# Kernel optimization log

Hardware: AMD Instinct MI355X
Metric: run time of the kernel (lower is better)

## Reference

```python
import jax, jax.numpy as jnp
import numpy as np

NUM_HEADS = 32
HEAD_DIM = 128
HIDDEN = 4096
MAX_SEQ = 4096
B, S = 8, 16
POS = 2048


def setup_inputs() -> dict:
    key = jax.random.key(0)
    ks = jax.random.split(key, 7)
    sc = 1.0 / np.sqrt(HIDDEN)
    return {
        "h": jax.random.normal(ks[0], (B, S, HIDDEN), dtype=jnp.float32),
        "Wq": jax.random.normal(ks[1], (HIDDEN, HIDDEN), dtype=jnp.float32) * sc,
        "Wk": jax.random.normal(ks[2], (HIDDEN, HIDDEN), dtype=jnp.float32) * sc,
        "Wv": jax.random.normal(ks[3], (HIDDEN, HIDDEN), dtype=jnp.float32) * sc,
        "Wo": jax.random.normal(ks[4], (HIDDEN, HIDDEN), dtype=jnp.float32) * sc,
        "K_cache": jax.random.normal(ks[5], (B, NUM_HEADS, MAX_SEQ, HEAD_DIM), dtype=jnp.float32),
        "V_cache": jax.random.normal(ks[6], (B, NUM_HEADS, MAX_SEQ, HEAD_DIM), dtype=jnp.float32),
        "pos": POS,
    }


def reference(h, Wq, Wk, Wv, Wo, K_cache, V_cache, pos):
    b, s, _ = h.shape
    # QKV projections (Linear with weight [out, in], no bias): h @ W.T
    def proj(W):
        return (h @ W.T).reshape(b, s, NUM_HEADS, HEAD_DIM).transpose(0, 2, 1, 3)  # [B,H,S,hd]
    Q, K, V = proj(Wq), proj(Wk), proj(Wv)
    # write new K/V into cache at [pos : pos+S] (pos is a static Python int)
    K_cache = K_cache.at[:, :, pos:pos + s, :].set(K)
    V_cache = V_cache.at[:, :, pos:pos + s, :].set(V)
    K_all = K_cache[:, :, :pos + s, :]  # [B,H,T,hd], T = pos+S
    V_all = V_cache[:, :, :pos + s, :]
    scores = jnp.einsum('bhsd,bhtd->bhst', Q, K_all) / np.sqrt(HEAD_DIM)  # [B,H,S,T]
    if s > 1:
        # causal mask applied only to the freshly-written block of columns
        causal = jnp.triu(jnp.full((s, s), -jnp.inf, dtype=scores.dtype), k=1)
        scores = scores.at[:, :, :, pos:pos + s].add(causal)
    attn = jax.nn.softmax(scores, axis=-1)
    out = jnp.einsum('bhst,bhtd->bhsd', attn, V_all)  # [B,H,S,hd]
    out = out.transpose(0, 2, 1, 3).reshape(b, s, NUM_HEADS * HEAD_DIM)
    return out @ Wo.T
```

## Files before the change

kernel.cpp:

```cpp
#include <hip/hip_runtime.h>

typedef _Float16 f16;
typedef _Float16 f16x8 __attribute__((ext_vector_type(8)));
typedef _Float16 f16x4 __attribute__((ext_vector_type(4)));
typedef _Float16 f16x2 __attribute__((ext_vector_type(2)));
typedef float f32x4 __attribute__((ext_vector_type(4)));
typedef float f32x2 __attribute__((ext_vector_type(2)));

#define MFMA16(a, b, c) __builtin_amdgcn_mfma_f32_16x16x32_f16(a, b, c, 0, 0, 0)

#define HID 4096
#define ROWS 128
#define SCL 0.12751743f

__device__ __forceinline__ f16x8 cvt8(float4 x, float4 y) {
    f16x8 v = {(f16)x.x, (f16)x.y, (f16)x.z, (f16)x.w,
               (f16)y.x, (f16)y.y, (f16)y.z, (f16)y.w};
    return v;
}

__device__ __forceinline__ int swz2(int row, int cb) {
    return row * 256 + (cb ^ ((row & 7) << 4));
}

__global__ void k_cvt(const float* __restrict__ src, f16* __restrict__ dst) {
    const int i = blockIdx.x * blockDim.x + threadIdx.x;
    const float4* s4 = (const float4*)src + (size_t)i * 2;
    float4 x = s4[0], y = s4[1];
    *((f16x8*)dst + i) = cvt8(x, y);
}

__global__ __launch_bounds__(256) void k_qproj(
        const f16* __restrict__ hb, const float* __restrict__ W,
        f16* __restrict__ Ob) {
    const int c0 = blockIdx.x * 16;

    __shared__ __align__(16) f16 sA[128 * 128];
    __shared__ __align__(16) f16 sB[16 * 128];

    const int tid = threadIdx.x;
    const int w = tid >> 6, l = tid & 63;
    const int rw = w * 32;
    const int ar = tid >> 4;
    const int ac = (tid & 15) * 8;

    f32x4 acc0 = {}, acc1 = {};

    float4 wx, wy;
    f16x8 hreg[8];
    {
        const float* wp = W + (size_t)(c0 + ar) * HID + ac;
        wx = *(const float4*)wp; wy = *(const float4*)(wp + 4);
        #pragma unroll
        for (int c = 0; c < 8; ++c)
            hreg[c] = *(const f16x8*)(hb + (size_t)(c * 16 + ar) * HID + ac);
    }

    for (int ks = 0; ks < 32; ++ks) {
        #pragma unroll
        for (int c = 0; c < 8; ++c)
            *(f16x8*)((char*)sA + swz2(c * 16 + ar, ac * 2)) = hreg[c];
        *(f16x8*)((char*)sB + swz2(ar, ac * 2)) = cvt8(wx, wy);
        __syncthreads();
        if (ks < 31) {
            const int k0 = (ks + 1) * 128;
            const float* wp = W + (size_t)(c0 + ar) * HID + k0 + ac;
            wx = *(const float4*)wp; wy = *(const float4*)(wp + 4);
            #pragma unroll
            for (int c = 0; c < 8; ++c)
                hreg[c] = *(const f16x8*)(hb + (size_t)(c * 16 + ar) * HID + k0 + ac);
        }
        #pragma unroll
        for (int kk = 0; kk < 4; ++kk) {
            const int cb = kk * 64 + (l >> 4) * 16;
            f16x8 a0 = *(const f16x8*)((char*)sA + swz2(rw + (l & 15), cb));
            f16x8 a1 = *(const f16x8*)((char*)sA + swz2(rw + 16 + (l & 15), cb));
            f16x8 b0 = *(const f16x8*)((char*)sB + swz2((l & 15), cb));
            acc0 = MFMA16(a0, b0, acc0);
            acc1 = MFMA16(a1, b0, acc1);
        }
        __syncthreads();
    }
    #pragma unroll
    for (int r = 0; r < 4; ++r) {
        const int col = c0 + (l & 15);
        Ob[(size_t)(rw + (l >> 4) * 4 + r) * HID + col]      = (f16)acc0[r];
        Ob[(size_t)(rw + 16 + (l >> 4) * 4 + r) * HID + col] = (f16)acc1[r];
    }
}

__global__ __launch_bounds__(512) void k_mega(
        const f16* __restrict__ hb,
        const float* __restrict__ Wk, const float* __restrict__ Wv,
        f16* __restrict__ Kw, f16* __restrict__ Vw,
        const f16* __restrict__ Qw,
        const float* __restrict__ Kc, const float* __restrict__ Vc,
        const int* __restrict__ posp,
        float* __restrict__ Pm, float* __restrict__ Pl, float* __restrict__ Po) {

    __shared__ __align__(16) char smem[65536 + 1024];
    const int tid = threadIdx.x, w = tid >> 6, l = tid & 63;

    if (blockIdx.x & 1) {
        const int pid = blockIdx.x >> 1;
        const float* __restrict__ W = (pid & 128) ? Wv : Wk;
        f16* __restrict__ Ob = (pid & 128) ? Vw : Kw;
        const int c0 = (pid & 127) * 32;

        f16* sA = (f16*)smem;
        f16* sB = (f16*)smem + 128 * 128;

        const int ar = tid >> 4;
        const int ac = (tid & 15) * 8;

        f32x4 acc0 = {}, acc1 = {};

        float4 wx, wy;
        f16x8 hreg[4];
        {
            const float* wp = W + (size_t)(c0 + ar) * HID + ac;
            wx = *(const float4*)wp; wy = *(const float4*)(wp + 4);
            #pragma unroll
            for (int c = 0; c < 4; ++c)
                hreg[c] = *(const f16x8*)(hb + (size_t)(c * 32 + ar) * HID + ac);
        }

        const int rw = (w >> 1) * 32;
        const int cw = (w & 1) * 16;

        for (int ks = 0; ks < 32; ++ks) {
            #pragma unroll
            for (int c = 0; c < 4; ++c)
                *(f16x8*)((char*)sA + swz2(c * 32 + ar, ac * 2)) = hreg[c];
            *(f16x8*)((char*)sB + swz2(ar, ac * 2)) = cvt8(wx, wy);
            __syncthreads();
            if (ks < 31) {
                const int k0 = (ks + 1) * 128;
                const float* wp = W + (size_t)(c0 + ar) * HID + k0 + ac;
                wx = *(const float4*)wp; wy = *(const float4*)(wp + 4);
                #pragma unroll
                for (int c = 0; c < 4; ++c)
                    hreg[c] = *(const f16x8*)(hb + (size_t)(c * 32 + ar) * HID + k0 + ac);
            }
            #pragma unroll
            for (int kk = 0; kk < 4; ++kk) {
                const int cb = kk * 64 + (l >> 4) * 16;
                f16x8 a0 = *(const f16x8*)((char*)sA + swz2(rw + (l & 15), cb));
                f16x8 a1 = *(const f16x8*)((char*)sA + swz2(rw + 16 + (l & 15), cb));
                f16x8 b0 = *(const f16x8*)((char*)sB + swz2(cw + (l & 15), cb));
                acc0 = MFMA16(a0, b0, acc0);
                acc1 = MFMA16(a1, b0, acc1);
            }
            __syncthreads();
        }
        #pragma unroll
        for (int r = 0; r < 4; ++r) {
            const int col = c0 + cw + (l & 15);
            Ob[(size_t)(rw + (l >> 4) * 4 + r) * HID + col]      = (f16)acc0[r];
            Ob[(size_t)(rw + 16 + (l >> 4) * 4 + r) * HID + col] = (f16)acc1[r];
        }
        return;
    }

    const int bh = blockIdx.x >> 1;
    const int b = bh >> 5, hh = bh & 31;
    const int pos = *posp;
    const int npure = pos >> 5;

    const float* Kb = Kc + (size_t)bh * (4096 * 128);
    const float* Vb = Vc + (size_t)bh * (4096 * 128);

    f16x8 qf[4];
    {
        const f16* qp = Qw + (size_t)(b * 16 + (l & 15)) * HID + hh * 128 + (l >> 4) * 8;
        #pragma unroll
        for (int kk = 0; kk < 4; ++kk) qf[kk] = *(const f16x8*)(qp + kk * 32);
    }

    f32x4 o[8] = {};
    float m[4], lsum[4];
    #pragma unroll
    for (int r = 0; r < 4; ++r) { m[r] = -3e38f; lsum[r] = 0.f; }

    f16* Pw = (f16*)smem + w * 640;

    const int start = (w * npure) >> 3;
    const int end   = ((w + 1) * npure) >> 3;
    for (int tau = start; tau < end; ++tau) {
        const int t0 = tau << 5;

        f16x8 kf[2][4];
        #pragma unroll
        for (int tn = 0; tn < 2; ++tn) {
            const float* kp = Kb + (size_t)(t0 + tn * 16 + (l & 15)) * 128 + (l >> 4) * 8;
            #pragma unroll
            for (int kk = 0; kk < 4; ++kk) {
                float4 x = *(const float4*)(kp + kk * 32);
                float4 y = *(const float4*)(kp + kk * 32 + 4);
                kf[tn][kk] = cvt8(x, y);
            }
        }
        f32x4 sa[2] = {};
        #pragma unroll
        for (int tn = 0; tn < 2; ++tn)
            #pragma unroll
            for (int kk = 0; kk < 4; ++kk) sa[tn] = MFMA16(qf[kk], kf[tn][kk], sa[tn]);

        f16x8 vf[8];
        {
            const float* vp = Vb + (size_t)(t0 + (l >> 4) * 8) * 128 + (l & 15);
            #pragma unroll
            for (int dt = 0; dt < 8; ++dt)
                #pragma unroll
                for (int j = 0; j < 8; ++j) vf[dt][j] = (f16)vp[j * 128 + dt * 16];
        }

        float sc[2][4];
        #pragma unroll
        for (int tn = 0; tn < 2; ++tn)
            #pragma unroll
            for (int r = 0; r < 4; ++r) sc[tn][r] = sa[tn][r] * SCL;
        float vmax[4];
        #pragma unroll
        for (int r = 0; r < 4; ++r) vmax[r] = fmaxf(sc[0][r], sc[1][r]);
        #pragma unroll
        for (int d = 1; d < 16; d <<= 1)
            #pragma unroll
            for (int r = 0; r < 4; ++r) vmax[r] = fmaxf(vmax[r], __shfl_xor(vmax[r], d));
        float p[2][4], rs[4], fac[4];
        #pragma unroll
        for (int r = 0; r < 4; ++r) {
            const float mn = fmaxf(m[r], vmax[r]);
            fac[r] = exp2f(m[r] - mn);
            m[r] = mn;
            p[0][r] = exp2f(sc[0][r] - mn);
            p[1][r] = exp2f(sc[1][r] - mn);
            rs[r] = p[0][r] + p[1][r];
            lsum[r] *= fac[r];
        }
        #pragma unroll
        for (int d = 1; d < 16; d <<= 1)
            #pragma unroll
            for (int r = 0; r < 4; ++r) rs[r] += __shfl_xor(rs[r], d);
        #pragma unroll
        for (int r = 0; r < 4; ++r) lsum[r] += rs[r];
        #pragma unroll
        for (int dt = 0; dt < 8; ++dt)
            #pragma unroll
            for (int r = 0; r < 4; ++r) o[dt][r] *= fac[r];

        #pragma unroll
        for (int r = 0; r < 4; ++r) {
            const int s_ = (l >> 4) * 4 + r;
            Pw[s_ * 40 + (l & 15)]      = (f16)p[0][r];
            Pw[s_ * 40 + 16 + (l & 15)] = (f16)p[1][r];
        }
        asm volatile("s_waitcnt lgkmcnt(0)" ::: "memory");
        f16x8 pa = *(const f16x8*)(Pw + (l & 15) * 40 + (l >> 4) * 8);

        #pragma unroll
        for (int dt = 0; dt < 8; ++dt) o[dt] = MFMA16(pa, vf[dt], o[dt]);
    }

    __syncthreads();
    float* Osh = (float*)smem;
    float* Msh = (float*)(smem + 65536);
    float* Lsh = Msh + 128;
    #pragma unroll
    for (int dt = 0; dt < 8; ++dt)
        #pragma unroll
        for (int r = 0; r < 4; ++r)
            Osh[w * 2048 + ((l >> 4) * 4 + r) * 128 + dt * 16 + (l & 15)] = o[dt][r];
    if ((l & 15) == 0) {
        #pragma unroll
        for (int r = 0; r < 4; ++r) {
            Msh[w * 16 + (l >> 4) * 4 + r] = m[r];
            Lsh[w * 16 + (l >> 4) * 4 + r] = lsum[r];
        }
    }
    __syncthreads();
    {
        const int s_ = tid >> 5;
        const int d_ = (tid & 31) * 4;
        float M = -3e38f;
        #pragma unroll
        for (int ww = 0; ww < 8; ++ww) M = fmaxf(M, Msh[ww * 16 + s_]);
        float L = 0.f;
        f32x4 oa = {};
        #pragma unroll
        for (int ww = 0; ww < 8; ++ww) {
            const float e = exp2f(Msh[ww * 16 + s_] - M);
            L += e * Lsh[ww * 16 + s_];
            f32x4 v = *(const f32x4*)(Osh + ww * 2048 + s_ * 128 + d_);
            #pragma unroll
            for (int r = 0; r < 4; ++r) oa[r] += e * v[r];
        }
        if ((tid & 31) == 0) {
            Pm[bh * 16 + s_] = M;
            Pl[bh * 16 + s_] = L;
        }
        *(f32x4*)(Po + (size_t)bh * 2048 + s_ * 128 + d_) = oa;
    }
}

__global__ __launch_bounds__(256) void k_fin(
        const f16* __restrict__ Qw, const f16* __restrict__ Kw,
        const f16* __restrict__ Vw,
        const float* __restrict__ Kc, const float* __restrict__ Vc,
        const int* __restrict__ posp,
        const float* __restrict__ Pm, const float* __restrict__ Pl,
        const float* __restrict__ Po, f16* __restrict__ Ow) {

    __shared__ float sP[16][48];
    __shared__ float sF[16], sL[16];

    const int bh = blockIdx.x, b = bh >> 5, hh = bh & 31;
    const int tid = threadIdx.x;
    const int pos = *posp;
    const int base = (pos >> 5) << 5;
    const int nb = pos + 16 - base;

    {
        const int s_ = tid >> 4, tt0 = tid & 15;
        const f16* qp = Qw + (size_t)(b * 16 + s_) * HID + hh * 128;
        const float m_p = Pm[bh * 16 + s_];
        const float l_p = Pl[bh * 16 + s_];

        float sc[3];
        float rowmax = -3e38f;
        #pragma unroll
        for (int it = 0; it < 3; ++it) {
            const int tt = it * 16 + tt0;
            float d = -3e38f;
            if (tt < nb) {
                const int t = base + tt;
                float acc = 0.f;
                if (t < pos) {
                    const float* kp = Kc + ((size_t)bh * 4096 + t) * 128;
                    #pragma unroll
                    for (int c = 0; c < 16; ++c) {
                        f16x8 q8 = *(const f16x8*)(qp + c * 8);
                        float4 ka = *(const float4*)(kp + c * 8);
                        float4 kb = *(const float4*)(kp + c * 8 + 4);
                        acc += (float)q8[0] * ka.x + (float)q8[1] * ka.y +
                               (float)q8[2] * ka.z + (float)q8[3] * ka.w +
                               (float)q8[4] * kb.x + (float)q8[5] * kb.y +
                               (float)q8[6] * kb.z + (float)q8[7] * kb.w;
                    }
                    d = acc * SCL;
                } else {
                    const f16* kp = Kw + (size_t)(b * 16 + (t - pos)) * HID + hh * 128;
                    #pragma unroll
                    for (int c = 0; c < 16; ++c) {
                        f16x8 q8 = *(const f16x8*)(qp + c * 8);
                        f16x8 k8 = *(const f16x8*)(kp + c * 8);
                        #pragma unroll
                        for (int j = 0; j < 8; ++j) acc += (float)q8[j] * (float)k8[j];
                    }
                    d = acc * SCL;
                    if ((t - pos) > s_) d = -3e38f;
                }
            }
            sc[it] = d;
            rowmax = fmaxf(rowmax, d);
        }
        #pragma unroll
        for (int dd = 1; dd < 16; dd <<= 1)
            rowmax = fmaxf(rowmax, __shfl_xor(rowmax, dd));

        const float M = fmaxf(m_p, rowmax);
        const float fac = exp2f(m_p - M);
        float ps = 0.f;
        #pragma unroll
        for (int it = 0; it < 3; ++it) {
            const float p = (sc[it] < -1e29f) ? 0.f : exp2f(sc[it] - M);
            ps += p;
            sP[s_][it * 16 + tt0] = p;
        }
        #pragma unroll
        for (int dd = 1; dd < 16; dd <<= 1) ps += __shfl_xor(ps, dd);
        if (tt0 == 0) {
            sF[s_] = fac;
            sL[s_] = fac * l_p + ps;
        }
    }
    __syncthreads();

    {
        const int s2 = tid >> 4;
        const int d0 = (tid & 15) * 8;
        const float f = sF[s2];
        float acc[8];
        const float* po = Po + (size_t)bh * 2048 + s2 * 128 + d0;
        #pragma unroll
        for (int j = 0; j < 8; ++j) acc[j] = f * po[j];

        for (int tt = 0; tt < nb; ++tt) {
            const float pv = sP[s2][tt];
            const int t = base + tt;
            if (t < pos) {
                const float* vp = Vc + ((size_t)bh * 4096 + t) * 128 + d0;
                float4 va = *(const float4*)vp;
                float4 vb = *(const float4*)(vp + 4);
                acc[0] += pv * va.x; acc[1] += pv * va.y;
                acc[2] += pv * va.z; acc[3] += pv * va.w;
                acc[4] += pv * vb.x; acc[5] += pv * vb.y;
                acc[6] += pv * vb.z; acc[7] += pv * vb.w;
            } else {
                const f16* vp = Vw + (size_t)(b * 16 + (t - pos)) * HID + hh * 128 + d0;
                f16x8 v8 = *(const f16x8*)vp;
                #pragma unroll
                for (int j = 0; j < 8; ++j) acc[j] += pv * (float)v8[j];
            }
        }
        const float inv = 1.f / sL[s2];
        f16x8 res;
        #pragma unroll
        for (int j = 0; j < 8; ++j) res[j] = (f16)(acc[j] * inv);
        *(f16x8*)(Ow + (size_t)(b * 16 + s2) * HID + hh * 128 + d0) = res;
    }
}

__global__ __launch_bounds__(256) void k_oproj(
        const f16* __restrict__ Oa, const float* __restrict__ Wo,
        float* __restrict__ out) {
    const int c0 = blockIdx.x * 16;

    __shared__ __align__(16) f16 sA[128 * 128];
    __shared__ __align__(16) f16 sB[16 * 128];

    const int tid = threadIdx.x;
    const int w = tid >> 6, l = tid & 63;
    const int rw = w * 32;
    const int ar = tid >> 4;
    const int ac = (tid & 15) * 8;

    f32x4 acc0 = {}, acc1 = {};

    float4 wx, wy;
    f16x8 hreg[8];
    {
        const float* wp = Wo + (size_t)(c0 + ar) * HID + ac;
        wx = *(const float4*)wp; wy = *(const float4*)(wp + 4);
        #pragma unroll
        for (int c = 0; c < 8; ++c)
            hreg[c] = *(const f16x8*)(Oa + (size_t)(c * 16 + ar) * HID + ac);
    }

    for (int ks = 0; ks < 32; ++ks) {
        #pragma unroll
        for (int c = 0; c < 8; ++c)
            *(f16x8*)((char*)sA + swz2(c * 16 + ar, ac * 2)) = hreg[c];
        *(f16x8*)((char*)sB + swz2(ar, ac * 2)) = cvt8(wx, wy);
        __syncthreads();
        if (ks < 31) {
            const int k0 = (ks + 1) * 128;
            const float* wp = Wo + (size_t)(c0 + ar) * HID + k0 + ac;
            wx = *(const float4*)wp; wy = *(const float4*)(wp + 4);
            #pragma unroll
            for (int c = 0; c < 8; ++c)
                hreg[c] = *(const f16x8*)(Oa + (size_t)(c * 16 + ar) * HID + k0 + ac);
        }
        #pragma unroll
        for (int kk = 0; kk < 4; ++kk) {
            const int cb = kk * 64 + (l >> 4) * 16;
            f16x8 a0 = *(const f16x8*)((char*)sA + swz2(rw + (l & 15), cb));
            f16x8 a1 = *(const f16x8*)((char*)sA + swz2(rw + 16 + (l & 15), cb));
            f16x8 b0 = *(const f16x8*)((char*)sB + swz2((l & 15), cb));
            acc0 = MFMA16(a0, b0, acc0);
            acc1 = MFMA16(a1, b0, acc1);
        }
        __syncthreads();
    }
    #pragma unroll
    for (int r = 0; r < 4; ++r) {
        const int col = c0 + (l & 15);
        out[(size_t)(rw + (l >> 4) * 4 + r) * HID + col]      = acc0[r];
        out[(size_t)(rw + 16 + (l >> 4) * 4 + r) * HID + col] = acc1[r];
    }
}

extern "C" void kernel_launch(void* const* d_in, const int* in_sizes, int n_in,
                              void* d_out, int out_size, void* d_ws, size_t ws_size,
                              hipStream_t stream) {
    const float* h  = (const float*)d_in[0];
    const float* Wq = (const float*)d_in[1];
    const float* Wk = (const float*)d_in[2];
    const float* Wv = (const float*)d_in[3];
    const float* Wo = (const float*)d_in[4];
    const float* Kc = (const float*)d_in[5];
    const float* Vc = (const float*)d_in[6];
    const int* pos  = (const int*)d_in[7];
    float* out = (float*)d_out;

    f16* hws = (f16*)d_ws;
    f16* Qw  = hws + ROWS * HID;
    f16* Kw  = Qw + ROWS * HID;
    f16* Vw  = Kw + ROWS * HID;
    f16* Ow  = Vw + ROWS * HID;
    float* Pm = (float*)(Ow + ROWS * HID);
    float* Pl = Pm + 256 * 16;
    float* Po = Pl + 256 * 16;

    k_cvt<<<256, 256, 0, stream>>>(h, hws);
    k_qproj<<<256, 256, 0, stream>>>(hws, Wq, Qw);
    k_mega<<<512, 512, 0, stream>>>(hws, Wk, Wv, Kw, Vw, Qw, Kc, Vc, pos, Pm, Pl, Po);
    k_fin<<<256, 256, 0, stream>>>(Qw, Kw, Vw, Kc, Vc, pos, Pm, Pl, Po, Ow);
    k_oproj<<<256, 256, 0, stream>>>(Ow, Wo, out);
}
```

Before: 229.1 us.

## Split K/V projection out of attention kernel and split attention over two blocks per head

The fused mega kernel, which interleaved K/V projection blocks with attention blocks, is split into two kernels. A single projection kernel now computes Q, K and V with 768 blocks. The attention kernel now gives each (batch, head) two blocks, each covering half of the cached sequence, and writes two partial softmax states. The finishing kernel merges both partials with rescaling. This spreads the cache-streaming attention across twice as many blocks, at the cost of an extra kernel boundary and a serial dependency between projection and attention.

```diff
diff --git a/kernel.cpp b/kernel.cpp
--- a/kernel.cpp
+++ b/kernel.cpp
@@ -30,10 +30,16 @@
     *((f16x8*)dst + i) = cvt8(x, y);
 }
 
-__global__ __launch_bounds__(256) void k_qproj(
-        const f16* __restrict__ hb, const float* __restrict__ W,
-        f16* __restrict__ Ob) {
-    const int c0 = blockIdx.x * 16;
+__global__ __launch_bounds__(256) void k_proj(
+        const f16* __restrict__ hb,
+        const float* __restrict__ Wq, const float* __restrict__ Wk,
+        const float* __restrict__ Wv,
+        f16* __restrict__ Qw, f16* __restrict__ Kw, f16* __restrict__ Vw) {
+    const int mat = blockIdx.x >> 8;
+    const int ct  = blockIdx.x & 255;
+    const float* __restrict__ W = (mat == 0) ? Wq : (mat == 1) ? Wk : Wv;
+    f16* __restrict__ Ob = (mat == 0) ? Qw : (mat == 1) ? Kw : Vw;
+    const int c0 = ct * 16;
 
     __shared__ __align__(16) f16 sA[128 * 128];
     __shared__ __align__(16) f16 sB[16 * 128];
@@ -89,83 +95,22 @@
     }
 }
 
-__global__ __launch_bounds__(512) void k_mega(
-        const f16* __restrict__ hb,
-        const float* __restrict__ Wk, const float* __restrict__ Wv,
-        f16* __restrict__ Kw, f16* __restrict__ Vw,
+__global__ __launch_bounds__(512) void k_attn(
         const f16* __restrict__ Qw,
         const float* __restrict__ Kc, const float* __restrict__ Vc,
         const int* __restrict__ posp,
         float* __restrict__ Pm, float* __restrict__ Pl, float* __restrict__ Po) {
 
     __shared__ __align__(16) char smem[65536 + 1024];
+
+    const int bh = blockIdx.x >> 1;
+    const int q  = blockIdx.x & 1;
+    const int b = bh >> 5, hh = bh & 31;
     const int tid = threadIdx.x, w = tid >> 6, l = tid & 63;
-
-    if (blockIdx.x & 1) {
-        const int pid = blockIdx.x >> 1;
-        const float* __restrict__ W = (pid & 128) ? Wv : Wk;
-        f16* __restrict__ Ob = (pid & 128) ? Vw : Kw;
-        const int c0 = (pid & 127) * 32;
-
-        f16* sA = (f16*)smem;
-        f16* sB = (f16*)smem + 128 * 128;
-
-        const int ar = tid >> 4;
-        const int ac = (tid & 15) * 8;
-
-        f32x4 acc0 = {}, acc1 = {};
-
-        float4 wx, wy;
-        f16x8 hreg[4];
-        {
-            const float* wp = W + (size_t)(c0 + ar) * HID + ac;
-            wx = *(const float4*)wp; wy = *(const float4*)(wp + 4);
-            #pragma unroll
-            for (int c = 0; c < 4; ++c)
-                hreg[c] = *(const f16x8*)(hb + (size_t)(c * 32 + ar) * HID + ac);
-        }
-
-        const int rw = (w >> 1) * 32;
-        const int cw = (w & 1) * 16;
-
-        for (int ks = 0; ks < 32; ++ks) {
-            #pragma unroll
-            for (int c = 0; c < 4; ++c)
-                *(f16x8*)((char*)sA + swz2(c * 32 + ar, ac * 2)) = hreg[c];
-            *(f16x8*)((char*)sB + swz2(ar, ac * 2)) = cvt8(wx, wy);
-            __syncthreads();
-            if (ks < 31) {
-                const int k0 = (ks + 1) * 128;
-                const float* wp = W + (size_t)(c0 + ar) * HID + k0 + ac;
-                wx = *(const float4*)wp; wy = *(const float4*)(wp + 4);
-                #pragma unroll
-                for (int c = 0; c < 4; ++c)
-                    hreg[c] = *(const f16x8*)(hb + (size_t)(c * 32 + ar) * HID + k0 + ac);
-            }
-            #pragma unroll
-            for (int kk = 0; kk < 4; ++kk) {
-                const int cb = kk * 64 + (l >> 4) * 16;
-                f16x8 a0 = *(const f16x8*)((char*)sA + swz2(rw + (l & 15), cb));
-                f16x8 a1 = *(const f16x8*)((char*)sA + swz2(rw + 16 + (l & 15), cb));
-                f16x8 b0 = *(const f16x8*)((char*)sB + swz2(cw + (l & 15), cb));
-                acc0 = MFMA16(a0, b0, acc0);
-                acc1 = MFMA16(a1, b0, acc1);
-            }
-            __syncthreads();
-        }
-        #pragma unroll
-        for (int r = 0; r < 4; ++r) {
-            const int col = c0 + cw + (l & 15);
-            Ob[(size_t)(rw + (l >> 4) * 4 + r) * HID + col]      = (f16)acc0[r];
-            Ob[(size_t)(rw + 16 + (l >> 4) * 4 + r) * HID + col] = (f16)acc1[r];
-        }
-        return;
-    }
-
-    const int bh = blockIdx.x >> 1;
-    const int b = bh >> 5, hh = bh & 31;
     const int pos = *posp;
     const int npure = pos >> 5;
+    const int nblk = npure >> 1;
+    const int tbase = q * nblk;
 
     const float* Kb = Kc + (size_t)bh * (4096 * 128);
     const float* Vb = Vc + (size_t)bh * (4096 * 128);
@@ -184,8 +129,8 @@
 
     f16* Pw = (f16*)smem + w * 640;
 
-    const int start = (w * npure) >> 3;
-    const int end   = ((w + 1) * npure) >> 3;
+    const int start = tbase + ((w * nblk) >> 3);
+    const int end   = tbase + (((w + 1) * nblk) >> 3);
     for (int tau = start; tau < end; ++tau) {
         const int t0 = tau << 5;
 
@@ -280,6 +225,7 @@
     }
     __syncthreads();
     {
+        const int pb = blockIdx.x;
         const int s_ = tid >> 5;
         const int d_ = (tid & 31) * 4;
         float M = -3e38f;
@@ -296,10 +242,10 @@
             for (int r = 0; r < 4; ++r) oa[r] += e * v[r];
         }
         if ((tid & 31) == 0) {
-            Pm[bh * 16 + s_] = M;
-            Pl[bh * 16 + s_] = L;
-        }
-        *(f32x4*)(Po + (size_t)bh * 2048 + s_ * 128 + d_) = oa;
+            Pm[pb * 16 + s_] = M;
+            Pl[pb * 16 + s_] = L;
+        }
+        *(f32x4*)(Po + (size_t)pb * 2048 + s_ * 128 + d_) = oa;
     }
 }
 
@@ -312,7 +258,7 @@
         const float* __restrict__ Po, f16* __restrict__ Ow) {
 
     __shared__ float sP[16][48];
-    __shared__ float sF[16], sL[16];
+    __shared__ float sF0[16], sF1[16], sL[16];
 
     const int bh = blockIdx.x, b = bh >> 5, hh = bh & 31;
     const int tid = threadIdx.x;
@@ -323,8 +269,10 @@
     {
         const int s_ = tid >> 4, tt0 = tid & 15;
         const f16* qp = Qw + (size_t)(b * 16 + s_) * HID + hh * 128;
-        const float m_p = Pm[bh * 16 + s_];
-        const float l_p = Pl[bh * 16 + s_];
+        const float m0 = Pm[(bh * 2) * 16 + s_];
+        const float m1 = Pm[(bh * 2 + 1) * 16 + s_];
+        const float l0 = Pl[(bh * 2) * 16 + s_];
+        const float l1 = Pl[(bh * 2 + 1) * 16 + s_];
 
         float sc[3];
         float rowmax = -3e38f;
@@ -368,8 +316,9 @@
         for (int dd = 1; dd < 16; dd <<= 1)
             rowmax = fmaxf(rowmax, __shfl_xor(rowmax, dd));
 
-        const float M = fmaxf(m_p, rowmax);
-        const float fac = exp2f(m_p - M);
+        const float M = fmaxf(fmaxf(m0, m1), rowmax);
+        const float f0 = exp2f(m0 - M);
+        const float f1 = exp2f(m1 - M);
         float ps = 0.f;
         #pragma unroll
         for (int it = 0; it < 3; ++it) {
@@ -380,8 +329,9 @@
         #pragma unroll
         for (int dd = 1; dd < 16; dd <<= 1) ps += __shfl_xor(ps, dd);
         if (tt0 == 0) {
-            sF[s_] = fac;
-            sL[s_] = fac * l_p + ps;
+            sF0[s_] = f0;
+            sF1[s_] = f1;
+            sL[s_] = f0 * l0 + f1 * l1 + ps;
         }
     }
     __syncthreads();
@@ -389,11 +339,12 @@
     {
         const int s2 = tid >> 4;
         const int d0 = (tid & 15) * 8;
-        const float f = sF[s2];
+        const float f0 = sF0[s2], f1 = sF1[s2];
         float acc[8];
-        const float* po = Po + (size_t)bh * 2048 + s2 * 128 + d0;
-        #pragma unroll
-        for (int j = 0; j < 8; ++j) acc[j] = f * po[j];
+        const float* po0 = Po + (size_t)(bh * 2) * 2048 + s2 * 128 + d0;
+        const float* po1 = Po + (size_t)(bh * 2 + 1) * 2048 + s2 * 128 + d0;
+        #pragma unroll
+        for (int j = 0; j < 8; ++j) acc[j] = f0 * po0[j] + f1 * po1[j];
 
         for (int tt = 0; tt < nb; ++tt) {
             const float pv = sP[s2][tt];
@@ -499,12 +450,12 @@
     f16* Vw  = Kw + ROWS * HID;
     f16* Ow  = Vw + ROWS * HID;
     float* Pm = (float*)(Ow + ROWS * HID);
-    float* Pl = Pm + 256 * 16;
-    float* Po = Pl + 256 * 16;
+    float* Pl = Pm + 512 * 16;
+    float* Po = Pl + 512 * 16;
 
     k_cvt<<<256, 256, 0, stream>>>(h, hws);
-    k_qproj<<<256, 256, 0, stream>>>(hws, Wq, Qw);
-    k_mega<<<512, 512, 0, stream>>>(hws, Wk, Wv, Kw, Vw, Qw, Kc, Vc, pos, Pm, Pl, Po);
+    k_proj<<<768, 256, 0, stream>>>(hws, Wq, Wk, Wv, Qw, Kw, Vw);
+    k_attn<<<512, 512, 0, stream>>>(Qw, Kc, Vc, pos, Pm, Pl, Po);
     k_fin<<<256, 256, 0, stream>>>(Qw, Kw, Vw, Kc, Vc, pos, Pm, Pl, Po, Ow);
     k_oproj<<<256, 256, 0, stream>>>(Ow, Wo, out);
 }
```

Measured after the change: 218.7 us. 1.05x faster.
